# Kernel tuning notes

Hardware: AMD Instinct MI355X
Metric: run time of the kernel (lower is better)

## Reference

```python
import jax, jax.numpy as jnp
import numpy as np

TOP_K = 2
NUM_EXPERTS = 64
SEQ, BS, HS = 2048, 4, 4096
TOKENS = SEQ * BS  # tokens_per_batch
TOL = 1e-4
EPS = 1e-8


def sinkhorn(temp_cost):
    # temp_cost: (T, E) float32 logits. Mirrors SinkhornRouter.sinkhorn exactly.
    cost = jnp.exp(temp_cost)
    n0, n1 = cost.shape
    # initial d0 (overwritten inside loop in torch too, kept for fidelity of carry dtype/shape)
    d0 = (TOKENS / NUM_EXPERTS) * jnp.sum(jnp.exp(2.0 * temp_cost), axis=1)
    d1 = jnp.ones((n1,), dtype=cost.dtype)
    err0 = jnp.asarray(1e9, dtype=cost.dtype)

    def cond(carry):
        _, _, err = carry
        return err > TOL

    def body(carry):
        d0, d1, _ = carry  # d1 here plays the role of d1_old
        d0_new = (1.0 / n0) / (jnp.sum(d1 * cost, axis=1) + EPS)          # (T,)
        d1_new = (1.0 / n1) / (jnp.sum(d0_new[:, None] * cost, axis=0) + EPS)  # (E,)
        err = jnp.mean(jnp.abs(d1 - d1_new))
        return (d0_new, d1_new, err)

    d0, d1, _ = jax.lax.while_loop(cond, body, (d0, d1, err0))
    return d1 * cost * d0[:, None]


def setup_inputs() -> dict:
    key = jax.random.key(0)
    kx, kw = jax.random.split(key)
    x = jax.random.normal(kx, (SEQ, BS, HS), dtype=jnp.float32)
    W = jax.random.normal(kw, (NUM_EXPERTS, HS), dtype=jnp.float32) * 0.02
    return {"x": x, "W": W}


def reference(x, W):
    # router logits: (T, E)
    logits = jnp.reshape(x, (-1, x.shape[-1])) @ W.T
    # Sinkhorn normalization is done in fp32 under no_grad in torch -> stop_gradient
    norm_logits = sinkhorn(jax.lax.stop_gradient(logits).astype(jnp.float32))
    _, indices = jax.lax.top_k(norm_logits, TOP_K)  # (T, top_k) int32
    # top_k > 1 -> softmax activation (fp32, cast back)
    probs = jax.nn.softmax(logits.astype(jnp.float32), axis=-1).astype(logits.dtype)
    scores = jnp.take_along_axis(probs, indices, axis=1)  # (T, top_k)
    return scores, indices
```

## Files before the change

### kernel.cpp

```cpp
#include <hip/hip_runtime.h>
#include <hip/hip_cooperative_groups.h>
#include <math.h>

namespace cg = cooperative_groups;

namespace {
constexpr int kTokens = 8192;
constexpr int kHS = 4096;
constexpr float kTol = 1e-4f;
constexpr float kEps = 1e-8f;
constexpr int kMaxIters = 1000;
constexpr int kSinkBlocks = 64;
constexpr size_t kTagFloats = 128;
constexpr size_t kGdataFloats = 2 * 64 * 64;
constexpr size_t kLogitsOff = kTagFloats + kGdataFloats;
constexpr size_t kLogitsFloats = (size_t)kTokens * 64;
constexpr size_t kWhiOff = kLogitsOff + kLogitsFloats;
constexpr size_t kWFragFloats = (size_t)(kHS / 32) * 4 * 64 * 4;
constexpr size_t kWloOff = kWhiOff + kWFragFloats;
constexpr size_t kWsNeedFloats = kWloOff + kWFragFloats;
constexpr size_t kWtpFloats = (size_t)(kHS / 4) * 64 * 4;
}

__device__ __forceinline__ float wave_sum(float v) {
#pragma unroll
  for (int o = 32; o; o >>= 1) v += __shfl_xor(v, o, 64);
  return v;
}

typedef __attribute__((ext_vector_type(8))) short bf16x8;
typedef __attribute__((ext_vector_type(4))) float f32x4;

__device__ __forceinline__ unsigned short f2bf(float x) {
  unsigned u = __builtin_bit_cast(unsigned, x);
  u += 0x7fffu + ((u >> 16) & 1u);
  return (unsigned short)(u >> 16);
}

__device__ __forceinline__ void split8r(const float4 a, const float4 b,
                                        bf16x8& hi, bf16x8& lo) {
  const float v[8] = {a.x, a.y, a.z, a.w, b.x, b.y, b.z, b.w};
#pragma unroll
  for (int j = 0; j < 8; ++j) {
    const unsigned short h = f2bf(v[j]);
    const float hf = __builtin_bit_cast(float, (unsigned)h << 16);
    hi[j] = (short)h;
    lo[j] = (short)f2bf(v[j] - hf);
  }
}

__device__ __forceinline__ void split8(const float* p, bf16x8& hi, bf16x8& lo) {
  split8r(*(const float4*)p, *(const float4*)(p + 4), hi, lo);
}

__global__ void __launch_bounds__(256)
k_wsplit(const float* __restrict__ W, bf16x8* __restrict__ whi,
         bf16x8* __restrict__ wlo) {
  const int idx = blockIdx.x * 256 + threadIdx.x;
  const int lane = idx & 63;
  const int n = (idx >> 6) & 3;
  const int kk = idx >> 8;
  const int e = 16 * n + (lane & 15);
  const int k = kk * 32 + ((lane >> 4) << 3);
  bf16x8 hi, lo;
  split8(W + (size_t)e * kHS + k, hi, lo);
  whi[idx] = hi;
  wlo[idx] = lo;
}

__global__ void __launch_bounds__(512, 4)
k_logits(const float* __restrict__ X, const bf16x8* __restrict__ whi,
         const bf16x8* __restrict__ wlo, float* __restrict__ logits) {
  const int tid = threadIdx.x;
  const int lane = tid & 63;
  const int wid = tid >> 6;
  const int t0 = blockIdx.x * 16;
  const int r = lane & 15;
  const int g = lane >> 4;

  const float* xp = X + (size_t)(t0 + r) * kHS + wid * 512 + g * 8;
  const bf16x8* bh_base = whi + (size_t)wid * 16 * 4 * 64 + lane;
  const bf16x8* bl_base = wlo + (size_t)wid * 16 * 4 * 64 + lane;

  f32x4 acc[4];
#pragma unroll
  for (int n = 0; n < 4; ++n) acc[n] = (f32x4){0.f, 0.f, 0.f, 0.f};

#pragma unroll
  for (int c = 0; c < 4; ++c) {
    float4 xa[4][2];
#pragma unroll
    for (int i = 0; i < 4; ++i) {
      const float* p = xp + (size_t)(c * 4 + i) * 32;
      xa[i][0] = *(const float4*)p;
      xa[i][1] = *(const float4*)(p + 4);
    }
#pragma unroll
    for (int i = 0; i < 4; ++i) {
      const int ks = c * 4 + i;
      bf16x8 bh[4], bl[4];
#pragma unroll
      for (int n = 0; n < 4; ++n) {
        bh[n] = bh_base[(ks * 4 + n) * 64];
        bl[n] = bl_base[(ks * 4 + n) * 64];
      }
      bf16x8 ah, al;
      split8r(xa[i][0], xa[i][1], ah, al);
#pragma unroll
      for (int n = 0; n < 4; ++n) {
        acc[n] = __builtin_amdgcn_mfma_f32_16x16x32_bf16(ah, bh[n], acc[n],
                                                         0, 0, 0);
        acc[n] = __builtin_amdgcn_mfma_f32_16x16x32_bf16(al, bh[n], acc[n],
                                                         0, 0, 0);
        acc[n] = __builtin_amdgcn_mfma_f32_16x16x32_bf16(ah, bl[n], acc[n],
                                                         0, 0, 0);
      }
    }
  }

  __shared__ __align__(16) float red[8][16][68];
#pragma unroll
  for (int n = 0; n < 4; ++n)
#pragma unroll
    for (int q = 0; q < 4; ++q)
      red[wid][g * 4 + q][n * 16 + r] = acc[n][q];
  __syncthreads();

  const int t = tid >> 5;
  const int e2 = (tid & 31) * 2;
  float2 s = make_float2(0.f, 0.f);
#pragma unroll
  for (int w = 0; w < 8; ++w) {
    s.x += red[w][t][e2];
    s.y += red[w][t][e2 + 1];
  }
  *(float2*)(logits + (size_t)(t0 + t) * 64 + e2) = s;
}

__global__ void __launch_bounds__(1024, 1)
k_sinkhorn(const float* __restrict__ logits, float* __restrict__ out,
           unsigned* __restrict__ tags, float* __restrict__ gdata) {
  const int tid = threadIdx.x;
  const int lane = tid & 63;
  const int wid = __builtin_amdgcn_readfirstlane(tid >> 6);
  const int blk = blockIdx.x;
  __shared__ float lds[1024];

  const int t0 = blk * 128 + wid * 8;
  float lg[8], cst[8];
#pragma unroll
  for (int t = 0; t < 8; ++t) {
    const float a = logits[(size_t)(t0 + t) * 64 + lane];
    lg[t] = a;
    cst[t] = expf(a);
  }

  float d1 = 1.0f;
  float d0v[8];
  int buf = 0;
  for (int it = 0; it < kMaxIters; ++it) {
    float p = 0.0f;
#pragma unroll
    for (int t = 0; t < 8; ++t) {
      const float s = wave_sum(d1 * cst[t]);
      const float d0t = (1.0f / 8192.0f) / (s + kEps);
      d0v[t] = d0t;
      p = fmaf(d0t, cst[t], p);
    }
    __syncthreads();
    lds[wid * 64 + lane] = p;
    __syncthreads();
    const unsigned want = (unsigned)(it + 1);
    if (wid == 0) {
      float bp = 0.0f;
#pragma unroll
      for (int w = 0; w < 16; ++w) bp += lds[w * 64 + lane];
      __hip_atomic_store(&gdata[((size_t)buf * 64 + blk) * 64 + lane], bp,
                         __ATOMIC_RELAXED, __HIP_MEMORY_SCOPE_AGENT);
      __threadfence();
      if (lane == 0)
        __hip_atomic_store(&tags[buf * 64 + blk], want, __ATOMIC_RELEASE,
                           __HIP_MEMORY_SCOPE_AGENT);
      while (__hip_atomic_load(&tags[buf * 64 + lane], __ATOMIC_ACQUIRE,
                               __HIP_MEMORY_SCOPE_AGENT) != want) {
        __builtin_amdgcn_s_sleep(1);
      }
    }
    __syncthreads();
    float s2 = 0.0f;
#pragma unroll
    for (int i = 0; i < 4; ++i)
      s2 += __hip_atomic_load(
          &gdata[((size_t)buf * 64 + wid * 4 + i) * 64 + lane],
          __ATOMIC_RELAXED, __HIP_MEMORY_SCOPE_AGENT);
    lds[wid * 64 + lane] = s2;
    __syncthreads();
    float colsum = 0.0f;
#pragma unroll
    for (int w = 0; w < 16; ++w) colsum += lds[w * 64 + lane];
    const float d1n = (1.0f / 64.0f) / (colsum + kEps);
    const float err = wave_sum(fabsf(d1 - d1n)) * (1.0f / 64.0f);
    d1 = d1n;
    buf ^= 1;
    if (err <= kTol) break;
  }

#pragma unroll
  for (int t = 0; t < 8; ++t) {
    const float lgv = lg[t];
    float m = lgv;
#pragma unroll
    for (int o = 32; o; o >>= 1) m = fmaxf(m, __shfl_xor(m, o, 64));
    const float ex = expf(lgv - m);
    const float den = wave_sum(ex);
    const float prob = ex / den;

    const float v = (d1 * cst[t]) * d0v[t];
    float v1 = v;
    int i1 = lane;
#pragma unroll
    for (int o = 32; o; o >>= 1) {
      const float ov = __shfl_xor(v1, o, 64);
      const int oi = __shfl_xor(i1, o, 64);
      if (ov > v1 || (ov == v1 && oi < i1)) { v1 = ov; i1 = oi; }
    }
    float v2 = (lane == i1) ? -INFINITY : v;
    int i2 = lane;
#pragma unroll
    for (int o = 32; o; o >>= 1) {
      const float ov = __shfl_xor(v2, o, 64);
      const int oi = __shfl_xor(i2, o, 64);
      if (ov > v2 || (ov == v2 && oi < i2)) { v2 = ov; i2 = oi; }
    }
    const float p1 = __shfl(prob, i1, 64);
    const float p2 = __shfl(prob, i2, 64);
    if (lane == 0) {
      const int row = t0 + t;
      out[row * 2 + 0] = p1;
      out[row * 2 + 1] = p2;
      out[2 * kTokens + row * 2 + 0] = (float)i1;
      out[2 * kTokens + row * 2 + 1] = (float)i2;
    }
  }
}

__global__ void __launch_bounds__(256, 1)
sinkhorn_router(const float* __restrict__ X, const float* __restrict__ W,
                float* __restrict__ out, float* __restrict__ ws) {
  cg::grid_group grid = cg::this_grid();
  const int tid = threadIdx.x;
  const int lane = tid & 63;
  const int wid = __builtin_amdgcn_readfirstlane(tid >> 6);
  const int blk = blockIdx.x;

  float4* wtp = reinterpret_cast<float4*>(ws);
  float* gpart = ws + kWtpFloats;
  __shared__ float lds[256];

  {
    const int j = blk * 256 + tid;
    const int e = j & 63;
    const int k4 = j >> 6;
    wtp[j] = *reinterpret_cast<const float4*>(W + (size_t)e * kHS + 4 * (size_t)k4);
  }
  grid.sync();

  const int t0 = blk * 32 + wid * 8;
  const float* xb = X + (size_t)t0 * kHS;
  float lg[8];
#pragma unroll
  for (int t = 0; t < 8; ++t) lg[t] = 0.0f;

#pragma unroll 2
  for (int k4 = 0; k4 < kHS / 4; ++k4) {
    const float4 w = wtp[k4 * 64 + lane];
#pragma unroll
    for (int t = 0; t < 8; ++t) {
      const float* xr = xb + (size_t)t * kHS + 4 * (size_t)k4;
      float a = lg[t];
      a = fmaf(xr[0], w.x, a);
      a = fmaf(xr[1], w.y, a);
      a = fmaf(xr[2], w.z, a);
      a = fmaf(xr[3], w.w, a);
      lg[t] = a;
    }
  }

  float cst[8];
#pragma unroll
  for (int t = 0; t < 8; ++t) cst[t] = expf(lg[t]);

  float d1 = 1.0f;
  float d0v[8];
  int buf = 0;
  for (int it = 0; it < kMaxIters; ++it) {
    float p = 0.0f;
#pragma unroll
    for (int t = 0; t < 8; ++t) {
      const float s = wave_sum(d1 * cst[t]);
      const float d0t = (1.0f / 8192.0f) / (s + kEps);
      d0v[t] = d0t;
      p = fmaf(d0t, cst[t], p);
    }
    __syncthreads();
    lds[wid * 64 + lane] = p;
    __syncthreads();
    if (wid == 0) {
      const float bp =
          lds[lane] + lds[64 + lane] + lds[128 + lane] + lds[192 + lane];
      gpart[buf * (256 * 64) + blk * 64 + lane] = bp;
    }
    grid.sync();
    const float* gp = gpart + buf * (256 * 64);
    float s = 0.0f;
#pragma unroll 8
    for (int b = 0; b < 64; ++b) s += gp[(wid * 64 + b) * 64 + lane];
    lds[wid * 64 + lane] = s;
    __syncthreads();
    const float colsum =
        lds[lane] + lds[64 + lane] + lds[128 + lane] + lds[192 + lane];
    const float d1n = (1.0f / 64.0f) / (colsum + kEps);
    const float err = wave_sum(fabsf(d1 - d1n)) * (1.0f / 64.0f);
    d1 = d1n;
    buf ^= 1;
    if (err <= kTol) break;
  }

#pragma unroll
  for (int t = 0; t < 8; ++t) {
    const float lgv = lg[t];
    float m = lgv;
#pragma unroll
    for (int o = 32; o; o >>= 1) m = fmaxf(m, __shfl_xor(m, o, 64));
    const float ex = expf(lgv - m);
    const float den = wave_sum(ex);
    const float prob = ex / den;

    const float v = (d1 * cst[t]) * d0v[t];
    float v1 = v;
    int i1 = lane;
#pragma unroll
    for (int o = 32; o; o >>= 1) {
      const float ov = __shfl_xor(v1, o, 64);
      const int oi = __shfl_xor(i1, o, 64);
      if (ov > v1 || (ov == v1 && oi < i1)) { v1 = ov; i1 = oi; }
    }
    float v2 = (lane == i1) ? -INFINITY : v;
    int i2 = lane;
#pragma unroll
    for (int o = 32; o; o >>= 1) {
      const float ov = __shfl_xor(v2, o, 64);
      const int oi = __shfl_xor(i2, o, 64);
      if (ov > v2 || (ov == v2 && oi < i2)) { v2 = ov; i2 = oi; }
    }
    const float p1 = __shfl(prob, i1, 64);
    const float p2 = __shfl(prob, i2, 64);
    if (lane == 0) {
      const int row = t0 + t;
      out[row * 2 + 0] = p1;
      out[row * 2 + 1] = p2;
      out[2 * kTokens + row * 2 + 0] = (float)i1;
      out[2 * kTokens + row * 2 + 1] = (float)i2;
    }
  }
}

extern "C" void kernel_launch(void* const* d_in, const int* in_sizes, int n_in,
                              void* d_out, int out_size, void* d_ws,
                              size_t ws_size, hipStream_t stream) {
  const float* X = (const float*)d_in[0];
  const float* W = (const float*)d_in[1];
  float* out = (float*)d_out;
  float* ws = (float*)d_ws;

  const size_t need = kWsNeedFloats * sizeof(float);
  if (ws_size < need) {
    void* args[] = {(void*)&X, (void*)&W, (void*)&out, (void*)&ws};
    hipLaunchCooperativeKernel((const void*)sinkhorn_router, dim3(256),
                               dim3(256), args, 0, stream);
    return;
  }

  unsigned* tags = reinterpret_cast<unsigned*>(ws);
  float* gdata = ws + kTagFloats;
  float* logits = ws + kLogitsOff;
  bf16x8* whi = reinterpret_cast<bf16x8*>(ws + kWhiOff);
  bf16x8* wlo = reinterpret_cast<bf16x8*>(ws + kWloOff);

  hipLaunchKernelGGL(k_wsplit, dim3((kHS / 32) * 4 * 64 / 256), dim3(256), 0,
                     stream, W, whi, wlo);
  hipLaunchKernelGGL(k_logits, dim3(kTokens / 16), dim3(512), 0, stream, X,
                     whi, wlo, logits);
  hipLaunchKernelGGL(k_sinkhorn, dim3(kSinkBlocks), dim3(1024), 0, stream,
                     logits, out, tags, gdata);
}
```

Baseline: 248.4 us.

## Split logits GEMM along K across four blocks and sum partials in sinkhorn

The logits kernel now divides the hidden dimension into four slices, each handled by its own 256-thread block, so the grid grows from 512 to 2048 blocks. Each block writes a partial 16x64 result, and the sinkhorn kernel adds the four partials as it loads logits. The X loads are also software-pipelined two k-steps ahead. The aim is more parallelism and better latency hiding in the memory-bound GEMM, at the cost of four times the partial-logit writes and extra reads in sinkhorn.

```diff
diff --git a/kernel.cpp b/kernel.cpp
--- a/kernel.cpp
+++ b/kernel.cpp
@@ -11,11 +11,12 @@
 constexpr float kEps = 1e-8f;
 constexpr int kMaxIters = 1000;
 constexpr int kSinkBlocks = 64;
+constexpr int kSplit = 4;
 constexpr size_t kTagFloats = 128;
 constexpr size_t kGdataFloats = 2 * 64 * 64;
-constexpr size_t kLogitsOff = kTagFloats + kGdataFloats;
-constexpr size_t kLogitsFloats = (size_t)kTokens * 64;
-constexpr size_t kWhiOff = kLogitsOff + kLogitsFloats;
+constexpr size_t kPartOff = kTagFloats + kGdataFloats;
+constexpr size_t kPartFloats = (size_t)kTokens * kSplit * 64;
+constexpr size_t kWhiOff = kPartOff + kPartFloats;
 constexpr size_t kWFragFloats = (size_t)(kHS / 32) * 4 * 64 * 4;
 constexpr size_t kWloOff = kWhiOff + kWFragFloats;
 constexpr size_t kWsNeedFloats = kWloOff + kWFragFloats;
@@ -68,57 +69,62 @@
   wlo[idx] = lo;
 }
 
-__global__ void __launch_bounds__(512, 4)
+__global__ void __launch_bounds__(256, 5)
 k_logits(const float* __restrict__ X, const bf16x8* __restrict__ whi,
-         const bf16x8* __restrict__ wlo, float* __restrict__ logits) {
+         const bf16x8* __restrict__ wlo, float* __restrict__ part) {
   const int tid = threadIdx.x;
   const int lane = tid & 63;
   const int wid = tid >> 6;
-  const int t0 = blockIdx.x * 16;
+  const int tile = blockIdx.x >> 2;
+  const int sig = blockIdx.x & 3;
+  const int t0 = tile * 16;
   const int r = lane & 15;
   const int g = lane >> 4;
-
-  const float* xp = X + (size_t)(t0 + r) * kHS + wid * 512 + g * 8;
-  const bf16x8* bh_base = whi + (size_t)wid * 16 * 4 * 64 + lane;
-  const bf16x8* bl_base = wlo + (size_t)wid * 16 * 4 * 64 + lane;
+  const int kk0 = sig * 32 + wid * 8;
+
+  const float* xp = X + (size_t)(t0 + r) * kHS + kk0 * 32 + g * 8;
+  const bf16x8* bh_base = whi + (size_t)kk0 * 4 * 64 + lane;
+  const bf16x8* bl_base = wlo + (size_t)kk0 * 4 * 64 + lane;
 
   f32x4 acc[4];
 #pragma unroll
   for (int n = 0; n < 4; ++n) acc[n] = (f32x4){0.f, 0.f, 0.f, 0.f};
 
-#pragma unroll
-  for (int c = 0; c < 4; ++c) {
-    float4 xa[4][2];
-#pragma unroll
-    for (int i = 0; i < 4; ++i) {
-      const float* p = xp + (size_t)(c * 4 + i) * 32;
-      xa[i][0] = *(const float4*)p;
-      xa[i][1] = *(const float4*)(p + 4);
-    }
-#pragma unroll
-    for (int i = 0; i < 4; ++i) {
-      const int ks = c * 4 + i;
-      bf16x8 bh[4], bl[4];
-#pragma unroll
-      for (int n = 0; n < 4; ++n) {
-        bh[n] = bh_base[(ks * 4 + n) * 64];
-        bl[n] = bl_base[(ks * 4 + n) * 64];
-      }
-      bf16x8 ah, al;
-      split8r(xa[i][0], xa[i][1], ah, al);
-#pragma unroll
-      for (int n = 0; n < 4; ++n) {
-        acc[n] = __builtin_amdgcn_mfma_f32_16x16x32_bf16(ah, bh[n], acc[n],
-                                                         0, 0, 0);
-        acc[n] = __builtin_amdgcn_mfma_f32_16x16x32_bf16(al, bh[n], acc[n],
-                                                         0, 0, 0);
-        acc[n] = __builtin_amdgcn_mfma_f32_16x16x32_bf16(ah, bl[n], acc[n],
-                                                         0, 0, 0);
-      }
-    }
-  }
-
-  __shared__ __align__(16) float red[8][16][68];
+  float4 xa[2][2];
+  xa[0][0] = *(const float4*)(xp);
+  xa[0][1] = *(const float4*)(xp + 4);
+  xa[1][0] = *(const float4*)(xp + 32);
+  xa[1][1] = *(const float4*)(xp + 36);
+
+#pragma unroll
+  for (int ks = 0; ks < 8; ++ks) {
+    bf16x8 bh[4], bl[4];
+#pragma unroll
+    for (int n = 0; n < 4; ++n) {
+      bh[n] = bh_base[(ks * 4 + n) * 64];
+      bl[n] = bl_base[(ks * 4 + n) * 64];
+    }
+    const int cur = ks & 1;
+    const float4 x0 = xa[cur][0];
+    const float4 x1 = xa[cur][1];
+    if (ks + 2 < 8) {
+      xa[cur][0] = *(const float4*)(xp + (size_t)(ks + 2) * 32);
+      xa[cur][1] = *(const float4*)(xp + (size_t)(ks + 2) * 32 + 4);
+    }
+    bf16x8 ah, al;
+    split8r(x0, x1, ah, al);
+#pragma unroll
+    for (int n = 0; n < 4; ++n) {
+      acc[n] = __builtin_amdgcn_mfma_f32_16x16x32_bf16(ah, bh[n], acc[n],
+                                                       0, 0, 0);
+      acc[n] = __builtin_amdgcn_mfma_f32_16x16x32_bf16(al, bh[n], acc[n],
+                                                       0, 0, 0);
+      acc[n] = __builtin_amdgcn_mfma_f32_16x16x32_bf16(ah, bl[n], acc[n],
+                                                       0, 0, 0);
+    }
+  }
+
+  __shared__ __align__(16) float red[4][16][68];
 #pragma unroll
   for (int n = 0; n < 4; ++n)
 #pragma unroll
@@ -126,19 +132,19 @@
       red[wid][g * 4 + q][n * 16 + r] = acc[n][q];
   __syncthreads();
 
-  const int t = tid >> 5;
-  const int e2 = (tid & 31) * 2;
-  float2 s = make_float2(0.f, 0.f);
-#pragma unroll
-  for (int w = 0; w < 8; ++w) {
-    s.x += red[w][t][e2];
-    s.y += red[w][t][e2 + 1];
-  }
-  *(float2*)(logits + (size_t)(t0 + t) * 64 + e2) = s;
+  const int t = tid >> 4;
+  const int e4 = (tid & 15) * 4;
+  float4 s = *(const float4*)&red[0][t][e4];
+#pragma unroll
+  for (int w = 1; w < 4; ++w) {
+    const float4 p = *(const float4*)&red[w][t][e4];
+    s.x += p.x; s.y += p.y; s.z += p.z; s.w += p.w;
+  }
+  *(float4*)(part + ((size_t)(tile * 4 + sig) * 16 + t) * 64 + e4) = s;
 }
 
 __global__ void __launch_bounds__(1024, 1)
-k_sinkhorn(const float* __restrict__ logits, float* __restrict__ out,
+k_sinkhorn(const float* __restrict__ part, float* __restrict__ out,
            unsigned* __restrict__ tags, float* __restrict__ gdata) {
   const int tid = threadIdx.x;
   const int lane = tid & 63;
@@ -150,7 +156,10 @@
   float lg[8], cst[8];
 #pragma unroll
   for (int t = 0; t < 8; ++t) {
-    const float a = logits[(size_t)(t0 + t) * 64 + lane];
+    const int row = t0 + t;
+    const float* pb =
+        part + ((size_t)(row >> 4) * kSplit * 16 + (row & 15)) * 64 + lane;
+    const float a = pb[0] + pb[1024] + pb[2048] + pb[3072];
     lg[t] = a;
     cst[t] = expf(a);
   }
@@ -383,14 +392,14 @@
 
   unsigned* tags = reinterpret_cast<unsigned*>(ws);
   float* gdata = ws + kTagFloats;
-  float* logits = ws + kLogitsOff;
+  float* part = ws + kPartOff;
   bf16x8* whi = reinterpret_cast<bf16x8*>(ws + kWhiOff);
   bf16x8* wlo = reinterpret_cast<bf16x8*>(ws + kWloOff);
 
   hipLaunchKernelGGL(k_wsplit, dim3((kHS / 32) * 4 * 64 / 256), dim3(256), 0,
                      stream, W, whi, wlo);
-  hipLaunchKernelGGL(k_logits, dim3(kTokens / 16), dim3(512), 0, stream, X,
-                     whi, wlo, logits);
+  hipLaunchKernelGGL(k_logits, dim3((kTokens / 16) * kSplit), dim3(256), 0,
+                     stream, X, whi, wlo, part);
   hipLaunchKernelGGL(k_sinkhorn, dim3(kSinkBlocks), dim3(1024), 0, stream,
-                     logits, out, tags, gdata);
-}
+                     part, out, tags, gdata);
+}
```

New measurement: 261.0 us. 5.1% more time.
